# Kernel optimization log

Measured on AMD Instinct MI355X. Metric: run time of the kernel, lower is better.

Reference implementation:

```python
import jax, jax.numpy as jnp
import numpy as np

jax.config.update("jax_enable_x64", True)  # FixedPointMul math is done in float64, as in torch

B, S, H = 8, 4096, 768


def setup_inputs():
    key = jax.random.key(0)
    k = jax.random.split(key, 6)
    s_act = jnp.array([4.0 / 127.0], dtype=jnp.float32)  # per-tensor 8-bit activation scale

    def qact(kk):  # produce int8-quantized-looking activations
        x = jax.random.normal(kk, (B, S, H), jnp.float32)
        return s_act * jnp.clip(jnp.round(x / s_act), -128, 127)

    return {
        "hidden_states": qact(k[0]),
        "hidden_states_scaling_factor": s_act,
        "input_tensor": qact(k[1]),
        "input_tensor_scaling_factor": s_act,
        "dense_weight": 0.02 * jax.random.normal(k[2], (H, H), jnp.float32),
        "dense_bias": 0.01 * jax.random.normal(k[3], (H,), jnp.float32),
        "ln_weight": 1.0 + 0.05 * jax.random.normal(k[4], (H,), jnp.float32),
        "ln_bias": 0.05 * jax.random.normal(k[5], (H,), jnp.float32),
    }


def _sym_scale(k, smin, smax):
    n = 2 ** (k - 1) - 1
    return jnp.clip(jnp.maximum(jnp.abs(smin), jnp.abs(smax)), 1e-8, None) / n


def _sym_quant(x, k, scale):
    n = 2 ** (k - 1) - 1
    return jnp.clip(jnp.round(x / scale), -n, n - 1)


def _batch_frexp(x):
    # returns (round(mantissa * 2^31), 31 - exponent) as in ibert batch_frexp
    m, e = jnp.frexp(x)
    return jnp.floor(m * (2.0 ** 31) + 0.5), 31.0 - e


def _fixedpoint_mul(x, pre_scale, bit, z_scale, identity=None, id_scale=None):
    n = 2 ** (bit - 1) - 1
    ps = jnp.reshape(pre_scale, (1, 1, -1)).astype(jnp.float64)
    z = z_scale.astype(jnp.float64)
    z_int = jnp.round(x.astype(jnp.float64) / ps)
    m, e = _batch_frexp(ps / z)
    out = jnp.round(z_int * m / (2.0 ** e))
    if identity is not None:
        isf = jnp.reshape(id_scale, (1, 1, -1)).astype(jnp.float64)
        wx = jnp.round(identity.astype(jnp.float64) / isf)
        m1, e1 = _batch_frexp(isf / z)
        out = out + jnp.round(wx * m1 / (2.0 ** e1))
    return jnp.clip(out, -n - 1, n).astype(jnp.float32)


def _quant_act(x, bit, pre_scale, identity=None, id_scale=None):
    x_act = x if identity is None else x + identity
    s = _sym_scale(bit, x_act.min(), x_act.max())  # per-tensor scale (dynamic range)
    q = _fixedpoint_mul(x, pre_scale, bit, s, identity, id_scale)
    return q * s, s


def reference(hidden_states, hidden_states_scaling_factor, input_tensor, input_tensor_scaling_factor, dense_weight, dense_bias, ln_weight, ln_bias):
    # ---- QuantLinear: per-channel int8 weights, int32 bias ----
    w_min = dense_weight.min(axis=1)
    w_max = dense_weight.max(axis=1)
    fc_scale = _sym_scale(8, w_min, w_max)                      # [H_out]
    w_int = _sym_quant(dense_weight, 8, fc_scale[:, None])      # [H_out, H_in]
    bias_scale = fc_scale * hidden_states_scaling_factor        # [H_out]
    b_int = _sym_quant(dense_bias, 32, bias_scale)
    x_int = hidden_states / hidden_states_scaling_factor
    hs = (jnp.einsum("bsh,oh->bso", x_int, w_int) + b_int) * bias_scale
    # dropout: eval mode -> identity
    # ---- QuantAct(22-bit) with quantized residual add ----
    hs, ln_in_scale = _quant_act(hs, 22, bias_scale, input_tensor, input_tensor_scaling_factor)
    # ---- IntLayerNorm (integer-only LayerNorm) ----
    x_int = hs / ln_in_scale
    mean_int = jnp.round(jnp.mean(x_int, axis=2, keepdims=True))
    y_int = x_int - mean_int
    var0 = jnp.sum(y_int ** 2, axis=2, keepdims=True)
    shift = jnp.ceil(jnp.log2(jnp.sqrt(jnp.maximum(var0, 1.0) / 2.0 ** 32)))  # set_shift (max_bit=32)
    shift = jnp.maximum(0.0, shift.max())
    y_sh = jnp.floor(y_int / 2.0 ** shift)
    var_int = jnp.sum(y_sh ** 2, axis=2, keepdims=True)
    std_int = jnp.floor(jnp.sqrt(var_int)) * 2.0 ** shift
    factor = jnp.floor(2.0 ** 31 / std_int)
    y_int = jnp.floor(y_int * factor / 2.0)
    sf = jnp.sqrt(jnp.float32(H)) / 2.0 ** 30
    bias_int = jnp.floor((ln_bias / ln_weight) / sf)
    y_int = y_int + bias_int
    sf_out = sf * ln_weight                                     # [H]
    hs = y_int * sf_out
    # ---- QuantAct(8-bit) output requantization ----
    hs, out_scale = _quant_act(hs, 8, sf_out)
    return hs, out_scale
```

## Files before the change

### kernel.cpp

```cpp
#include <hip/hip_runtime.h>

typedef _Float16 half8 __attribute__((ext_vector_type(8)));
typedef _Float16 half4 __attribute__((ext_vector_type(4)));
typedef float f32x4 __attribute__((ext_vector_type(4)));

#define HDIM 768
#define NTOK 32768

static constexpr size_t WX_OFF   = 0;
static constexpr size_t WINT_OFF = 25165824;
static constexpr size_t RS1_OFF  = WINT_OFF + 1179648;
static constexpr size_t RS2_OFF  = RS1_OFF + 6144;
static constexpr size_t BS_OFF   = RS2_OFF + 6144;
static constexpr size_t BINT_OFF = BS_OFF + 3072;
static constexpr size_t LNBI_OFF = BINT_OFF + 3072;
static constexpr size_t SFO_OFF  = LNBI_OFF + 3072;
static constexpr size_t SC_OFF   = SFO_OFF + 3072;
static constexpr size_t RSM1_OFF = SC_OFF + 64;

__device__ __forceinline__ unsigned fenc(float f) {
    unsigned u = __float_as_uint(f);
    return (u >> 31) ? ~u : (u | 0x80000000u);
}
__device__ __forceinline__ float fdec(unsigned e) {
    unsigned u = (e >> 31) ? (e & 0x7fffffffu) : ~e;
    return __uint_as_float(u);
}

#define GLDS16(g, l) __builtin_amdgcn_global_load_lds( \
    (const __attribute__((address_space(1))) unsigned int*)(g), \
    (__attribute__((address_space(3))) unsigned int*)(l), 16, 0, 0)

__global__ __launch_bounds__(256) void k0_prep(const float* __restrict__ W,
                                               const float* __restrict__ bias,
                                               const float* __restrict__ ln_w,
                                               const float* __restrict__ ln_b,
                                               const float* __restrict__ phsf,
                                               char* __restrict__ ws) {
    int o = blockIdx.x, tid = threadIdx.x;
    __shared__ float red[256];
    __shared__ float fc_sh;
    float m = 0.f;
    for (int j = tid; j < HDIM; j += 256) m = fmaxf(m, fabsf(W[(size_t)o * HDIM + j]));
    red[tid] = m;
    __syncthreads();
    for (int s = 128; s; s >>= 1) { if (tid < s) red[tid] = fmaxf(red[tid], red[tid + s]); __syncthreads(); }
    if (tid == 0) {
        float fc = fmaxf(red[0], 1e-8f) / 127.0f;
        float hsf = *phsf;
        float bs = fc * hsf;
        fc_sh = fc;
        ((float*)(ws + BS_OFF))[o] = bs;
        ((int*)(ws + BINT_OFF))[o] = (int)rintf(bias[o] / bs);
        float sf = sqrtf(768.0f) / 1073741824.0f;
        float lw = ln_w[o], lb = ln_b[o];
        ((int*)(ws + LNBI_OFF))[o] = (int)floorf((lb / lw) / sf);
        ((float*)(ws + SFO_OFF))[o] = sf * lw;
    }
    __syncthreads();
    float fc = fc_sh;
    _Float16* w16 = (_Float16*)(ws + WINT_OFF);
    for (int j = tid; j < HDIM; j += 256) {
        float q = rintf(W[(size_t)o * HDIM + j] / fc);
        q = fminf(fmaxf(q, -127.f), 126.f);
        w16[(size_t)o * HDIM + j] = (_Float16)q;
    }
    if (blockIdx.x == 0 && tid < 8) {
        unsigned* sc = (unsigned*)(ws + SC_OFF);
        unsigned v = 0u;
        if (tid == 0 || tid == 2) v = 0xFFFFFFFFu;
        sc[tid] = v;
    }
}

#define BM 128
#define BN 128
#define BK 32
#define NKT (HDIM / BK)
__global__ __launch_bounds__(256) void k1_gemm(const float* __restrict__ hs_in,
                                               const float* __restrict__ inp,
                                               const float* __restrict__ phsf,
                                               const float* __restrict__ pisf,
                                               char* __restrict__ ws,
                                               int* __restrict__ accOut) {
    __shared__ _Float16 As[2][BM][BK + 8];
    __shared__ _Float16 Bs[2][4096];
    __shared__ float rmn[4], rmx[4];
    int tid = threadIdx.x;
    int lane = tid & 63, wave = tid >> 6;
    int wrow = lane & 15, wkg = lane >> 4;
    int bid = blockIdx.x;
    int xcd = bid & 7, slot = bid >> 3;
    int mtile = xcd * 32 + slot / 6;
    int ntile = slot % 6;
    int t0 = mtile * BM, o0 = ntile * BN;
    float inv_hsf = 1.0f / *phsf;
    float inv_isf = 1.0f / *pisf;
    const _Float16* w16 = (const _Float16*)(ws + WINT_OFF);

    int brow0 = tid >> 2,          bsub0 = (tid & 3) ^ (brow0 & 3);
    int brow1 = (256 + tid) >> 2,  bsub1 = ((256 + tid) & 3) ^ (brow1 & 3);
    const _Float16* bsrc0 = w16 + (size_t)(o0 + brow0) * HDIM + bsub0 * 8;
    const _Float16* bsrc1 = w16 + (size_t)(o0 + brow1) * HDIM + bsub1 * 8;
    int bofs0 = (0 * 256 + wave * 64) * 8;
    int bofs1 = (1 * 256 + wave * 64) * 8;

    int arow[4], acol4[4];
    #pragma unroll
    for (int i = 0; i < 4; ++i) { int c = i * 256 + tid; arow[i] = c >> 3; acol4[i] = c & 7; }

    GLDS16(bsrc0, &Bs[0][bofs0]);
    GLDS16(bsrc1, &Bs[0][bofs1]);
    {
        float4 av[4];
        #pragma unroll
        for (int i = 0; i < 4; ++i)
            av[i] = *(const float4*)(hs_in + (size_t)(t0 + arow[i]) * HDIM + acol4[i] * 4);
        #pragma unroll
        for (int i = 0; i < 4; ++i) {
            half4 h = { (_Float16)rintf(av[i].x * inv_hsf), (_Float16)rintf(av[i].y * inv_hsf),
                        (_Float16)rintf(av[i].z * inv_hsf), (_Float16)rintf(av[i].w * inv_hsf) };
            *(half4*)&As[0][arow[i]][acol4[i] * 4] = h;
        }
    }
    __syncthreads();

    int wm = wave & 1, wn = wave >> 1;
    f32x4 acc[4][4] = {};
    int aofs[4], bfofs[4];
    #pragma unroll
    for (int mi = 0; mi < 4; ++mi) aofs[mi] = wm * 64 + mi * 16 + wrow;
    #pragma unroll
    for (int nf = 0; nf < 4; ++nf) {
        int r = wn * 64 + nf * 16 + wrow;
        bfofs[nf] = (r * 4 + (wkg ^ (r & 3))) * 8;
    }

    for (int kt = 0; kt < NKT; ++kt) {
        int cur = kt & 1, nxt = 1 - cur;
        float4 av[4];
        if (kt < NKT - 1) {
            GLDS16(bsrc0 + (kt + 1) * BK, &Bs[nxt][bofs0]);
            GLDS16(bsrc1 + (kt + 1) * BK, &Bs[nxt][bofs1]);
            #pragma unroll
            for (int i = 0; i < 4; ++i)
                av[i] = *(const float4*)(hs_in + (size_t)(t0 + arow[i]) * HDIM + (kt + 1) * BK + acol4[i] * 4);
        }
        half8 af[4], bf[4];
        #pragma unroll
        for (int mi = 0; mi < 4; ++mi) af[mi] = *(const half8*)&As[cur][aofs[mi]][wkg * 8];
        #pragma unroll
        for (int nf = 0; nf < 4; ++nf) bf[nf] = *(const half8*)&Bs[cur][bfofs[nf]];
        #pragma unroll
        for (int mi = 0; mi < 4; ++mi)
            #pragma unroll
            for (int nf = 0; nf < 4; ++nf)
                acc[mi][nf] = __builtin_amdgcn_mfma_f32_16x16x32_f16(af[mi], bf[nf], acc[mi][nf], 0, 0, 0);
        if (kt < NKT - 1) {
            #pragma unroll
            for (int i = 0; i < 4; ++i) {
                half4 h = { (_Float16)rintf(av[i].x * inv_hsf), (_Float16)rintf(av[i].y * inv_hsf),
                            (_Float16)rintf(av[i].z * inv_hsf), (_Float16)rintf(av[i].w * inv_hsf) };
                *(half4*)&As[nxt][arow[i]][acol4[i] * 4] = h;
            }
            __syncthreads();
        }
    }

    const float* bscale = (const float*)(ws + BS_OFF);
    const int* bint = (const int*)(ws + BINT_OFF);
    char* wx = (char*)(ws + WX_OFF);
    float lmn = 3.402823466e38f, lmx = -3.402823466e38f;
    #pragma unroll
    for (int mi = 0; mi < 4; ++mi)
        #pragma unroll
        for (int nf = 0; nf < 4; ++nf) {
            int o = o0 + wn * 64 + nf * 16 + wrow;
            int bi = bint[o];
            float bsc = bscale[o];
            #pragma unroll
            for (int r = 0; r < 4; ++r) {
                int t = t0 + wm * 64 + mi * 16 + wkg * 4 + r;
                int a = (int)acc[mi][nf][r] + bi;
                size_t idx = (size_t)t * HDIM + o;
                accOut[idx] = a;
                float xin = inp[idx];
                float xa = (float)a * bsc + xin;
                lmn = fminf(lmn, xa);
                lmx = fmaxf(lmx, xa);
                wx[idx] = (char)rintf(xin * inv_isf);
            }
        }
    #pragma unroll
    for (int off = 32; off; off >>= 1) {
        lmn = fminf(lmn, __shfl_down(lmn, off));
        lmx = fmaxf(lmx, __shfl_down(lmx, off));
    }
    if (lane == 0) { rmn[wave] = lmn; rmx[wave] = lmx; }
    __syncthreads();
    if (tid == 0) {
        float mn = fminf(fminf(rmn[0], rmn[1]), fminf(rmn[2], rmn[3]));
        float mx = fmaxf(fmaxf(rmx[0], rmx[1]), fmaxf(rmx[2], rmx[3]));
        volatile unsigned* sc = (volatile unsigned*)(ws + SC_OFF);
        unsigned emn = fenc(mn), emx = fenc(mx);
        if (emn < sc[0]) atomicMin((unsigned*)&sc[0], emn);
        if (emx > sc[1]) atomicMax((unsigned*)&sc[1], emx);
    }
}

__global__ __launch_bounds__(256) void k2_scale1(const float* __restrict__ pisf, char* __restrict__ ws) {
    __shared__ float s_sh;
    unsigned* sc = (unsigned*)(ws + SC_OFF);
    if (threadIdx.x == 0) {
        float mn = fdec(sc[0]), mx = fdec(sc[1]);
        float s = fmaxf(fmaxf(fabsf(mn), fabsf(mx)), 1e-8f) / 2097151.0f;
        ((float*)sc)[5] = s;
        s_sh = s;
        double r = (double)(*pisf) / (double)s;
        int ex; double mant = frexp(r, &ex);
        double m1 = floor(mant * 2147483648.0 + 0.5);
        ((double*)(ws + RSM1_OFF))[0] = m1 * exp2((double)(ex - 31));
    }
    __syncthreads();
    float s = s_sh;
    const float* bs = (const float*)(ws + BS_OFF);
    double* rs1 = (double*)(ws + RS1_OFF);
    for (int o = threadIdx.x; o < HDIM; o += 256) {
        double r = (double)bs[o] / (double)s;
        int ex; double mant = frexp(r, &ex);
        double m = floor(mant * 2147483648.0 + 0.5);
        rs1[o] = m * exp2((double)(ex - 31));
    }
}

__global__ __launch_bounds__(256) void k3_rows(char* __restrict__ ws, int* __restrict__ buf) {
    int tid = threadIdx.x, lane = tid & 63, wave = tid >> 6;
    int wid = blockIdx.x * 4 + wave;
    const double* rs1 = (const double*)(ws + RS1_OFF);
    double rsm1 = *(const double*)(ws + RSM1_OFF);
    int localShift = 0;
    int4 aP[3]; int wP[3];
    {
        size_t b0 = (size_t)(wid * 4) * HDIM;
        #pragma unroll
        for (int c = 0; c < 3; ++c) {
            aP[c] = ((const int4*)(buf + b0))[lane + 64 * c];
            wP[c] = ((const int*)(ws + WX_OFF + b0))[lane + 64 * c];
        }
    }
    for (int rr = 0; rr < 4; ++rr) {
        int4 aN[3]; int wN[3];
        if (rr < 3) {
            size_t nb = (size_t)(wid * 4 + rr + 1) * HDIM;
            #pragma unroll
            for (int c = 0; c < 3; ++c) {
                aN[c] = ((const int4*)(buf + nb))[lane + 64 * c];
                wN[c] = ((const int*)(ws + WX_OFF + nb))[lane + 64 * c];
            }
        }
        size_t base = (size_t)(wid * 4 + rr) * HDIM;
        int q[12];
        int sum = 0;
        #pragma unroll
        for (int c = 0; c < 3; ++c) {
            int o0 = (lane + 64 * c) * 4;
            int av[4] = {aP[c].x, aP[c].y, aP[c].z, aP[c].w};
            #pragma unroll
            for (int j = 0; j < 4; ++j) {
                double q1 = rint((double)av[j] * rs1[o0 + j]);
                int wxj = (int)(char)(wP[c] >> (8 * j));
                double qq = q1 + rint((double)wxj * rsm1);
                qq = fmin(fmax(qq, -2097152.0), 2097151.0);
                q[c * 4 + j] = (int)qq;
                sum += q[c * 4 + j];
            }
        }
        #pragma unroll
        for (int off = 32; off; off >>= 1) sum += __shfl_xor(sum, off);
        int mean = (int)rint((double)sum / 768.0);
        long long var0 = 0;
        #pragma unroll
        for (int k = 0; k < 12; ++k) { q[k] -= mean; var0 += (long long)q[k] * (long long)q[k]; }
        #pragma unroll
        for (int off = 32; off; off >>= 1) var0 += __shfl_xor(var0, off);
        #pragma unroll
        for (int c = 0; c < 3; ++c) {
            int4 y = {q[c * 4 + 0], q[c * 4 + 1], q[c * 4 + 2], q[c * 4 + 3]};
            ((int4*)(buf + base))[lane + 64 * c] = y;
        }
        if (lane == 0) {
            double v = (double)(var0 < 1 ? 1LL : var0);
            int sr = (int)ceil(0.5 * log2(v) - 16.0);
            localShift = max(localShift, sr);
        }
        #pragma unroll
        for (int c = 0; c < 3; ++c) { aP[c] = aN[c]; wP[c] = wN[c]; }
    }
    if (lane == 0 && localShift > 0) {
        int* sp = (int*)(ws + SC_OFF) + 4;
        if (localShift > *(volatile int*)sp) atomicMax(sp, localShift);
    }
}

__global__ __launch_bounds__(256) void k4_rows(char* __restrict__ ws, int* __restrict__ buf) {
    int tid = threadIdx.x, lane = tid & 63, wave = tid >> 6;
    int wid = blockIdx.x * 4 + wave;
    int shift = *(((const int*)(ws + SC_OFF)) + 4);
    const int* lnbi = (const int*)(ws + LNBI_OFF);
    const float* sfo = (const float*)(ws + SFO_OFF);
    float lmn = 3.402823466e38f, lmx = -3.402823466e38f;
    int4 yP[3];
    {
        size_t b0 = (size_t)(wid * 4) * HDIM;
        #pragma unroll
        for (int c = 0; c < 3; ++c) yP[c] = ((const int4*)(buf + b0))[lane + 64 * c];
    }
    for (int rr = 0; rr < 4; ++rr) {
        int4 yN[3];
        if (rr < 3) {
            size_t nb = (size_t)(wid * 4 + rr + 1) * HDIM;
            #pragma unroll
            for (int c = 0; c < 3; ++c) yN[c] = ((const int4*)(buf + nb))[lane + 64 * c];
        }
        size_t base = (size_t)(wid * 4 + rr) * HDIM;
        int yv[12];
        #pragma unroll
        for (int c = 0; c < 3; ++c) {
            yv[c * 4 + 0] = yP[c].x; yv[c * 4 + 1] = yP[c].y; yv[c * 4 + 2] = yP[c].z; yv[c * 4 + 3] = yP[c].w;
        }
        long long var = 0;
        #pragma unroll
        for (int k = 0; k < 12; ++k) { int ysh = yv[k] >> shift; var += (long long)ysh * (long long)ysh; }
        #pragma unroll
        for (int off = 32; off; off >>= 1) var += __shfl_xor(var, off);
        double std_int = floor(sqrt((double)var)) * (double)(1LL << shift);
        if (std_int < 1.0) std_int = 1.0;
        long long factor = (long long)floor(2147483648.0 / std_int);
        #pragma unroll
        for (int c = 0; c < 3; ++c) {
            int o0 = (lane + 64 * c) * 4;
            int y2[4];
            #pragma unroll
            for (int j = 0; j < 4; ++j) {
                long long t = ((long long)yv[c * 4 + j] * factor) >> 1;
                int v2 = (int)t + lnbi[o0 + j];
                y2[j] = v2;
                float h = (float)v2 * sfo[o0 + j];
                lmn = fminf(lmn, h);
                lmx = fmaxf(lmx, h);
            }
            int4 w = {y2[0], y2[1], y2[2], y2[3]};
            ((int4*)(buf + base))[lane + 64 * c] = w;
        }
        #pragma unroll
        for (int c = 0; c < 3; ++c) yP[c] = yN[c];
    }
    #pragma unroll
    for (int off = 32; off; off >>= 1) {
        lmn = fminf(lmn, __shfl_xor(lmn, off));
        lmx = fmaxf(lmx, __shfl_xor(lmx, off));
    }
    if (lane == 0) {
        volatile unsigned* sc = (volatile unsigned*)(ws + SC_OFF);
        unsigned emn = fenc(lmn), emx = fenc(lmx);
        if (emn < sc[2]) atomicMin((unsigned*)&sc[2], emn);
        if (emx > sc[3]) atomicMax((unsigned*)&sc[3], emx);
    }
}

__global__ __launch_bounds__(256) void k5_scale2(char* __restrict__ ws) {
    __shared__ float s_sh;
    unsigned* sc = (unsigned*)(ws + SC_OFF);
    if (threadIdx.x == 0) {
        float mn = fdec(sc[2]), mx = fdec(sc[3]);
        float s2 = fmaxf(fmaxf(fabsf(mn), fabsf(mx)), 1e-8f) / 127.0f;
        ((float*)sc)[6] = s2;
        s_sh = s2;
    }
    __syncthreads();
    float s2 = s_sh;
    const float* sfo = (const float*)(ws + SFO_OFF);
    double* rs2 = (double*)(ws + RS2_OFF);
    for (int o = threadIdx.x; o < HDIM; o += 256) {
        double r = (double)sfo[o] / (double)s2;
        int ex; double mant = frexp(r, &ex);
        double m = floor(mant * 2147483648.0 + 0.5);
        rs2[o] = m * exp2((double)(ex - 31));
    }
}

__global__ __launch_bounds__(256) void k6_out(char* __restrict__ ws, float* __restrict__ out) {
    int idx4 = blockIdx.x * 256 + threadIdx.x;
    int4 y = ((const int4*)out)[idx4];
    const double* rs2 = (const double*)(ws + RS2_OFF);
    float s2 = ((const float*)(ws + SC_OFF))[6];
    int base = idx4 * 4;
    int o0 = base % HDIM;
    int yv[4] = {y.x, y.y, y.z, y.w};
    float4 r;
    float* rp = &r.x;
    #pragma unroll
    for (int j = 0; j < 4; ++j) {
        double q = rint((double)yv[j] * rs2[o0 + j]);
        q = fmin(fmax(q, -128.0), 127.0);
        rp[j] = (float)q * s2;
    }
    ((float4*)out)[idx4] = r;
    if (idx4 == 0) out[(size_t)NTOK * HDIM] = s2;
}

extern "C" void kernel_launch(void* const* d_in, const int* in_sizes, int n_in,
                              void* d_out, int out_size, void* d_ws, size_t ws_size,
                              hipStream_t stream) {
    const float* hs   = (const float*)d_in[0];
    const float* phsf = (const float*)d_in[1];
    const float* inp  = (const float*)d_in[2];
    const float* pisf = (const float*)d_in[3];
    const float* W    = (const float*)d_in[4];
    const float* bias = (const float*)d_in[5];
    const float* ln_w = (const float*)d_in[6];
    const float* ln_b = (const float*)d_in[7];
    char* ws = (char*)d_ws;
    float* out = (float*)d_out;
    int* buf = (int*)d_out;

    k0_prep<<<HDIM, 256, 0, stream>>>(W, bias, ln_w, ln_b, phsf, ws);
    k1_gemm<<<(NTOK / BM) * (HDIM / BN), 256, 0, stream>>>(hs, inp, phsf, pisf, ws, buf);
    k2_scale1<<<1, 256, 0, stream>>>(pisf, ws);
    k3_rows<<<NTOK / 16, 256, 0, stream>>>(ws, buf);
    k4_rows<<<NTOK / 16, 256, 0, stream>>>(ws, buf);
    k5_scale2<<<1, 256, 0, stream>>>(ws);
    k6_out<<<NTOK * HDIM / 1024, 256, 0, stream>>>(ws, out);
}
```

Measured before the change: 512.5 us.

## Switch GEMM to int8 MFMA with pre-quantized activations and direct-to-LDS loads

Adds a pre-pass that quantizes hidden states to int8 into the workspace, stores weights as int8, and runs the dense GEMM with i32_16x16x32_i8 MFMA using 128x192x64 tiles. Both operands are loaded with global_load_lds into a swizzled double buffer, with explicit waitcnt/barrier and setprio. The residual int8 quantization moves out of the GEMM epilogue into k3_rows, which now reads the float input directly. This halves operand bytes and doubles MFMA throughput relative to fp16. The cost is an extra pass over the activations and more float reads in k3.

```diff
diff --git a/kernel.cpp b/kernel.cpp
--- a/kernel.cpp
+++ b/kernel.cpp
@@ -1,8 +1,7 @@
 #include <hip/hip_runtime.h>
 
-typedef _Float16 half8 __attribute__((ext_vector_type(8)));
-typedef _Float16 half4 __attribute__((ext_vector_type(4)));
-typedef float f32x4 __attribute__((ext_vector_type(4)));
+typedef int   v4i   __attribute__((ext_vector_type(4)));
+typedef unsigned long u64x2 __attribute__((ext_vector_type(2)));
 
 #define HDIM 768
 #define NTOK 32768
@@ -30,6 +29,8 @@
 #define GLDS16(g, l) __builtin_amdgcn_global_load_lds( \
     (const __attribute__((address_space(1))) unsigned int*)(g), \
     (__attribute__((address_space(3))) unsigned int*)(l), 16, 0, 0)
+
+__device__ __forceinline__ int swz4(int r) { return (r & 3) ^ ((r >> 2) & 3); }
 
 __global__ __launch_bounds__(256) void k0_prep(const float* __restrict__ W,
                                                const float* __restrict__ bias,
@@ -59,11 +60,11 @@
     }
     __syncthreads();
     float fc = fc_sh;
-    _Float16* w16 = (_Float16*)(ws + WINT_OFF);
+    char* w8 = (char*)(ws + WINT_OFF);
     for (int j = tid; j < HDIM; j += 256) {
         float q = rintf(W[(size_t)o * HDIM + j] / fc);
         q = fminf(fmaxf(q, -127.f), 126.f);
-        w16[(size_t)o * HDIM + j] = (_Float16)q;
+        w8[(size_t)o * HDIM + j] = (char)q;
     }
     if (blockIdx.x == 0 && tid < 8) {
         unsigned* sc = (unsigned*)(ws + SC_OFF);
@@ -73,122 +74,135 @@
     }
 }
 
+__global__ __launch_bounds__(256) void kp_a8(const float* __restrict__ hs,
+                                             const float* __restrict__ phsf,
+                                             char* __restrict__ ws) {
+    int idx = blockIdx.x * 256 + threadIdx.x;
+    float inv = 1.0f / *phsf;
+    const float4* in4 = (const float4*)hs + (size_t)idx * 4;
+    unsigned ow[4];
+    #pragma unroll
+    for (int j = 0; j < 4; ++j) {
+        float4 v = in4[j];
+        int q0 = (int)rintf(v.x * inv), q1 = (int)rintf(v.y * inv);
+        int q2 = (int)rintf(v.z * inv), q3 = (int)rintf(v.w * inv);
+        ow[j] = (unsigned)(q0 & 255) | ((unsigned)(q1 & 255) << 8) |
+                ((unsigned)(q2 & 255) << 16) | ((unsigned)(q3 & 255) << 24);
+    }
+    ((uint4*)(ws + WX_OFF))[idx] = make_uint4(ow[0], ow[1], ow[2], ow[3]);
+}
+
 #define BM 128
-#define BN 128
-#define BK 32
+#define BN 192
+#define BK 64
 #define NKT (HDIM / BK)
-__global__ __launch_bounds__(256) void k1_gemm(const float* __restrict__ hs_in,
-                                               const float* __restrict__ inp,
-                                               const float* __restrict__ phsf,
-                                               const float* __restrict__ pisf,
+__global__ __launch_bounds__(256) void k1_gemm(const float* __restrict__ inp,
                                                char* __restrict__ ws,
                                                int* __restrict__ accOut) {
-    __shared__ _Float16 As[2][BM][BK + 8];
-    __shared__ _Float16 Bs[2][4096];
+    __shared__ alignas(16) char As[2][BM * BK];
+    __shared__ alignas(16) char Bs[2][BN * BK];
     __shared__ float rmn[4], rmx[4];
-    int tid = threadIdx.x;
-    int lane = tid & 63, wave = tid >> 6;
-    int wrow = lane & 15, wkg = lane >> 4;
+    int tid = threadIdx.x, lane = tid & 63, wave = tid >> 6;
+    int wrow = lane & 15, g = lane >> 4;
     int bid = blockIdx.x;
     int xcd = bid & 7, slot = bid >> 3;
-    int mtile = xcd * 32 + slot / 6;
-    int ntile = slot % 6;
+    int mtile = xcd * 32 + (slot >> 2);
+    int ntile = slot & 3;
     int t0 = mtile * BM, o0 = ntile * BN;
-    float inv_hsf = 1.0f / *phsf;
-    float inv_isf = 1.0f / *pisf;
-    const _Float16* w16 = (const _Float16*)(ws + WINT_OFF);
-
-    int brow0 = tid >> 2,          bsub0 = (tid & 3) ^ (brow0 & 3);
-    int brow1 = (256 + tid) >> 2,  bsub1 = ((256 + tid) & 3) ^ (brow1 & 3);
-    const _Float16* bsrc0 = w16 + (size_t)(o0 + brow0) * HDIM + bsub0 * 8;
-    const _Float16* bsrc1 = w16 + (size_t)(o0 + brow1) * HDIM + bsub1 * 8;
-    int bofs0 = (0 * 256 + wave * 64) * 8;
-    int bofs1 = (1 * 256 + wave * 64) * 8;
-
-    int arow[4], acol4[4];
-    #pragma unroll
-    for (int i = 0; i < 4; ++i) { int c = i * 256 + tid; arow[i] = c >> 3; acol4[i] = c & 7; }
-
-    GLDS16(bsrc0, &Bs[0][bofs0]);
-    GLDS16(bsrc1, &Bs[0][bofs1]);
-    {
-        float4 av[4];
-        #pragma unroll
-        for (int i = 0; i < 4; ++i)
-            av[i] = *(const float4*)(hs_in + (size_t)(t0 + arow[i]) * HDIM + acol4[i] * 4);
-        #pragma unroll
-        for (int i = 0; i < 4; ++i) {
-            half4 h = { (_Float16)rintf(av[i].x * inv_hsf), (_Float16)rintf(av[i].y * inv_hsf),
-                        (_Float16)rintf(av[i].z * inv_hsf), (_Float16)rintf(av[i].w * inv_hsf) };
-            *(half4*)&As[0][arow[i]][acol4[i] * 4] = h;
-        }
-    }
-    __syncthreads();
+    const char* a8 = (const char*)(ws + WX_OFF);
+    const char* w8 = (const char*)(ws + WINT_OFF);
+
+    const char* asrc[2]; const char* bsrc[3];
+    int aldso[2], bldso[3];
+    #pragma unroll
+    for (int i = 0; i < 2; ++i) {
+        int c = i * 256 + tid, r = c >> 2, s = c & 3;
+        asrc[i] = a8 + (size_t)(t0 + r) * HDIM + (s ^ swz4(r)) * 16;
+        aldso[i] = (i * 256 + wave * 64) * 16;
+    }
+    #pragma unroll
+    for (int i = 0; i < 3; ++i) {
+        int c = i * 256 + tid, r = c >> 2, s = c & 3;
+        bsrc[i] = w8 + (size_t)(o0 + r) * HDIM + (s ^ swz4(r)) * 16;
+        bldso[i] = (i * 256 + wave * 64) * 16;
+    }
 
     int wm = wave & 1, wn = wave >> 1;
-    f32x4 acc[4][4] = {};
-    int aofs[4], bfofs[4];
-    #pragma unroll
-    for (int mi = 0; mi < 4; ++mi) aofs[mi] = wm * 64 + mi * 16 + wrow;
-    #pragma unroll
-    for (int nf = 0; nf < 4; ++nf) {
-        int r = wn * 64 + nf * 16 + wrow;
-        bfofs[nf] = (r * 4 + (wkg ^ (r & 3))) * 8;
-    }
-
+    int aofs[4], bofs[6];
+    #pragma unroll
+    for (int mi = 0; mi < 4; ++mi) { int r = wm * 64 + mi * 16 + wrow; aofs[mi] = r * BK + ((g ^ swz4(r)) * 16); }
+    #pragma unroll
+    for (int nf = 0; nf < 6; ++nf) { int r = wn * 96 + nf * 16 + wrow; bofs[nf] = r * BK + ((g ^ swz4(r)) * 16); }
+
+    #pragma unroll
+    for (int i = 0; i < 2; ++i) GLDS16(asrc[i], &As[0][aldso[i]]);
+    #pragma unroll
+    for (int i = 0; i < 3; ++i) GLDS16(bsrc[i], &Bs[0][bldso[i]]);
+    #pragma unroll
+    for (int i = 0; i < 2; ++i) GLDS16(asrc[i] + BK, &As[1][aldso[i]]);
+    #pragma unroll
+    for (int i = 0; i < 3; ++i) GLDS16(bsrc[i] + BK, &Bs[1][bldso[i]]);
+    asm volatile("s_waitcnt vmcnt(5)" ::: "memory");
+    __builtin_amdgcn_s_barrier();
+
+    v4i acc[4][6] = {};
     for (int kt = 0; kt < NKT; ++kt) {
-        int cur = kt & 1, nxt = 1 - cur;
-        float4 av[4];
-        if (kt < NKT - 1) {
-            GLDS16(bsrc0 + (kt + 1) * BK, &Bs[nxt][bofs0]);
-            GLDS16(bsrc1 + (kt + 1) * BK, &Bs[nxt][bofs1]);
-            #pragma unroll
-            for (int i = 0; i < 4; ++i)
-                av[i] = *(const float4*)(hs_in + (size_t)(t0 + arow[i]) * HDIM + (kt + 1) * BK + acol4[i] * 4);
-        }
-        half8 af[4], bf[4];
-        #pragma unroll
-        for (int mi = 0; mi < 4; ++mi) af[mi] = *(const half8*)&As[cur][aofs[mi]][wkg * 8];
-        #pragma unroll
-        for (int nf = 0; nf < 4; ++nf) bf[nf] = *(const half8*)&Bs[cur][bfofs[nf]];
+        int cur = kt & 1;
+        u64x2 af[4], bf[6];
+        #pragma unroll
+        for (int mi = 0; mi < 4; ++mi) af[mi] = *(const u64x2*)&As[cur][aofs[mi]];
+        #pragma unroll
+        for (int nf = 0; nf < 6; ++nf) bf[nf] = *(const u64x2*)&Bs[cur][bofs[nf]];
+        asm volatile("s_waitcnt lgkmcnt(0)" ::: "memory");
+        __builtin_amdgcn_s_barrier();
+        if (kt + 2 < NKT) {
+            #pragma unroll
+            for (int i = 0; i < 2; ++i) GLDS16(asrc[i] + (kt + 2) * BK, &As[cur][aldso[i]]);
+            #pragma unroll
+            for (int i = 0; i < 3; ++i) GLDS16(bsrc[i] + (kt + 2) * BK, &Bs[cur][bldso[i]]);
+        }
+        __builtin_amdgcn_s_setprio(1);
         #pragma unroll
         for (int mi = 0; mi < 4; ++mi)
             #pragma unroll
-            for (int nf = 0; nf < 4; ++nf)
-                acc[mi][nf] = __builtin_amdgcn_mfma_f32_16x16x32_f16(af[mi], bf[nf], acc[mi][nf], 0, 0, 0);
-        if (kt < NKT - 1) {
-            #pragma unroll
-            for (int i = 0; i < 4; ++i) {
-                half4 h = { (_Float16)rintf(av[i].x * inv_hsf), (_Float16)rintf(av[i].y * inv_hsf),
-                            (_Float16)rintf(av[i].z * inv_hsf), (_Float16)rintf(av[i].w * inv_hsf) };
-                *(half4*)&As[nxt][arow[i]][acol4[i] * 4] = h;
+            for (int nf = 0; nf < 6; ++nf) {
+                acc[mi][nf] = __builtin_amdgcn_mfma_i32_16x16x32_i8((long)af[mi][0], (long)bf[nf][0], acc[mi][nf], 0, 0, 0);
+                acc[mi][nf] = __builtin_amdgcn_mfma_i32_16x16x32_i8((long)af[mi][1], (long)bf[nf][1], acc[mi][nf], 0, 0, 0);
             }
-            __syncthreads();
+        __builtin_amdgcn_s_setprio(0);
+        if (kt + 2 < NKT) {
+            asm volatile("s_waitcnt vmcnt(5)" ::: "memory");
+            __builtin_amdgcn_s_barrier();
+        } else if (kt + 2 == NKT) {
+            asm volatile("s_waitcnt vmcnt(0)" ::: "memory");
+            __builtin_amdgcn_s_barrier();
         }
     }
 
     const float* bscale = (const float*)(ws + BS_OFF);
     const int* bint = (const int*)(ws + BINT_OFF);
-    char* wx = (char*)(ws + WX_OFF);
+    int oo[6]; float bsc[6]; int bi[6];
+    #pragma unroll
+    for (int nf = 0; nf < 6; ++nf) {
+        oo[nf] = o0 + wn * 96 + nf * 16 + wrow;
+        bsc[nf] = bscale[oo[nf]];
+        bi[nf]  = bint[oo[nf]];
+    }
     float lmn = 3.402823466e38f, lmx = -3.402823466e38f;
     #pragma unroll
     for (int mi = 0; mi < 4; ++mi)
         #pragma unroll
-        for (int nf = 0; nf < 4; ++nf) {
-            int o = o0 + wn * 64 + nf * 16 + wrow;
-            int bi = bint[o];
-            float bsc = bscale[o];
-            #pragma unroll
-            for (int r = 0; r < 4; ++r) {
-                int t = t0 + wm * 64 + mi * 16 + wkg * 4 + r;
-                int a = (int)acc[mi][nf][r] + bi;
-                size_t idx = (size_t)t * HDIM + o;
+        for (int r = 0; r < 4; ++r) {
+            int t = t0 + wm * 64 + mi * 16 + g * 4 + r;
+            size_t rb = (size_t)t * HDIM;
+            #pragma unroll
+            for (int nf = 0; nf < 6; ++nf) {
+                int a = acc[mi][nf][r] + bi[nf];
+                size_t idx = rb + oo[nf];
                 accOut[idx] = a;
-                float xin = inp[idx];
-                float xa = (float)a * bsc + xin;
+                float xa = (float)a * bsc[nf] + inp[idx];
                 lmn = fminf(lmn, xa);
                 lmx = fmaxf(lmx, xa);
-                wx[idx] = (char)rintf(xin * inv_isf);
             }
         }
     #pragma unroll
@@ -233,29 +247,32 @@
     }
 }
 
-__global__ __launch_bounds__(256) void k3_rows(char* __restrict__ ws, int* __restrict__ buf) {
+__global__ __launch_bounds__(256) void k3_rows(char* __restrict__ ws, int* __restrict__ buf,
+                                               const float* __restrict__ inp,
+                                               const float* __restrict__ pisf) {
     int tid = threadIdx.x, lane = tid & 63, wave = tid >> 6;
     int wid = blockIdx.x * 4 + wave;
     const double* rs1 = (const double*)(ws + RS1_OFF);
     double rsm1 = *(const double*)(ws + RSM1_OFF);
+    float inv_isf = 1.0f / *pisf;
     int localShift = 0;
-    int4 aP[3]; int wP[3];
+    int4 aP[3]; float4 xP[3];
     {
         size_t b0 = (size_t)(wid * 4) * HDIM;
         #pragma unroll
         for (int c = 0; c < 3; ++c) {
             aP[c] = ((const int4*)(buf + b0))[lane + 64 * c];
-            wP[c] = ((const int*)(ws + WX_OFF + b0))[lane + 64 * c];
+            xP[c] = ((const float4*)(inp + b0))[lane + 64 * c];
         }
     }
     for (int rr = 0; rr < 4; ++rr) {
-        int4 aN[3]; int wN[3];
+        int4 aN[3]; float4 xN[3];
         if (rr < 3) {
             size_t nb = (size_t)(wid * 4 + rr + 1) * HDIM;
             #pragma unroll
             for (int c = 0; c < 3; ++c) {
                 aN[c] = ((const int4*)(buf + nb))[lane + 64 * c];
-                wN[c] = ((const int*)(ws + WX_OFF + nb))[lane + 64 * c];
+                xN[c] = ((const float4*)(inp + nb))[lane + 64 * c];
             }
         }
         size_t base = (size_t)(wid * 4 + rr) * HDIM;
@@ -265,10 +282,11 @@
         for (int c = 0; c < 3; ++c) {
             int o0 = (lane + 64 * c) * 4;
             int av[4] = {aP[c].x, aP[c].y, aP[c].z, aP[c].w};
+            float xv[4] = {xP[c].x, xP[c].y, xP[c].z, xP[c].w};
             #pragma unroll
             for (int j = 0; j < 4; ++j) {
                 double q1 = rint((double)av[j] * rs1[o0 + j]);
-                int wxj = (int)(char)(wP[c] >> (8 * j));
+                int wxj = (int)rintf(xv[j] * inv_isf);
                 double qq = q1 + rint((double)wxj * rsm1);
                 qq = fmin(fmax(qq, -2097152.0), 2097151.0);
                 q[c * 4 + j] = (int)qq;
@@ -294,7 +312,7 @@
             localShift = max(localShift, sr);
         }
         #pragma unroll
-        for (int c = 0; c < 3; ++c) { aP[c] = aN[c]; wP[c] = wN[c]; }
+        for (int c = 0; c < 3; ++c) { aP[c] = aN[c]; xP[c] = xN[c]; }
     }
     if (lane == 0 && localShift > 0) {
         int* sp = (int*)(ws + SC_OFF) + 4;
@@ -425,9 +443,10 @@
     int* buf = (int*)d_out;
 
     k0_prep<<<HDIM, 256, 0, stream>>>(W, bias, ln_w, ln_b, phsf, ws);
-    k1_gemm<<<(NTOK / BM) * (HDIM / BN), 256, 0, stream>>>(hs, inp, phsf, pisf, ws, buf);
+    kp_a8<<<NTOK * HDIM / 4096, 256, 0, stream>>>(hs, phsf, ws);
+    k1_gemm<<<(NTOK / BM) * (HDIM / BN), 256, 0, stream>>>(inp, ws, buf);
     k2_scale1<<<1, 256, 0, stream>>>(pisf, ws);
-    k3_rows<<<NTOK / 16, 256, 0, stream>>>(ws, buf);
+    k3_rows<<<NTOK / 16, 256, 0, stream>>>(ws, buf, inp, pisf);
     k4_rows<<<NTOK / 16, 256, 0, stream>>>(ws, buf);
     k5_scale2<<<1, 256, 0, stream>>>(ws);
     k6_out<<<NTOK * HDIM / 1024, 256, 0, stream>>>(ws, out);
```

Measured after the change: 440.1 us. 14.1% less time.
